# Optimization experiments

Measured on AMD Instinct MI355X. Metric: run time of the kernel, lower is better.

Reference implementation:

```python
import jax, jax.numpy as jnp
import numpy as np


def _pairwise_sq_dist(x, y):
    # x: [B, N, 3], y: [B, M, 3] -> P: [B, N, M] squared Euclidean distances
    xx = jnp.sum(x * x, axis=-1)                      # [B, N]
    yy = jnp.sum(y * y, axis=-1)                      # [B, M]
    zz = jnp.einsum('bnd,bmd->bnm', x, y)             # [B, N, M]
    return xx[:, :, None] + yy[:, None, :] - 2.0 * zz


def setup_inputs() -> dict:
    key = jax.random.key(0)
    k1, k2 = jax.random.split(key)
    B, K = 8, 8192
    adv_pc = jax.random.normal(k1, (B, K, 3), dtype=jnp.float32)
    ori_pc = jax.random.normal(k2, (B, K, 3), dtype=jnp.float32)
    weights = jnp.ones((B,), dtype=jnp.float32)
    return {"adv_pc": adv_pc, "ori_pc": ori_pc, "weights": weights}


def reference(adv_pc, ori_pc, weights):
    # P = pairwise_dist(gts=ori_pc, preds=adv_pc): [B, N_ori, N_adv]
    P = _pairwise_sq_dist(ori_pc, adv_pc)
    # method='adv2ori': loss1 = max over adv points of min over ori points
    loss1 = jnp.max(jnp.min(P, axis=1), axis=1)       # [B]
    loss = loss1 * weights
    return jnp.mean(loss)                             # batch_avg=True
```

## Files before the change

kernel.cpp:

```cpp
#include <hip/hip_runtime.h>


#define KPTS 8192
#define BATCH 8
#define NSPLIT 8
#define RBLK (KPTS / NSPLIT)
#define TSLICE (RBLK / 32)
#define CBLK 512
#define MCHUNK (KPTS / CBLK)

typedef _Float16 half8 __attribute__((ext_vector_type(8)));

#define TILE_ASM(af_, rm0_, rm1_, rm2_, rm3_, b0_, b1_, b2_, b3_)             \
    asm volatile(                                                             \
        "v_mfma_f32_32x32x16_f16 v[64:79], %4, %5, 0\n\t"                     \
        "v_mfma_f32_32x32x16_f16 v[80:95], %4, %6, 0\n\t"                     \
        "v_mfma_f32_32x32x16_f16 v[96:111], %4, %7, 0\n\t"                    \
        "v_mfma_f32_32x32x16_f16 v[112:127], %4, %8, 0\n\t"                   \
        "s_nop 7\n\t"                                                         \
        "s_nop 7\n\t"                                                         \
        "v_min3_f32 v64, v64, v65, v66\n\t"                                   \
        "v_min3_f32 v67, v67, v68, v69\n\t"                                   \
        "v_min3_f32 v70, v70, v71, v72\n\t"                                   \
        "v_min3_f32 v73, v73, v74, v75\n\t"                                   \
        "v_min3_f32 v76, v76, v77, v78\n\t"                                   \
        "v_min3_f32 v79, v79, %0, v64\n\t"                                    \
        "v_min3_f32 v67, v67, v70, v73\n\t"                                   \
        "v_min3_f32 %0, v76, v79, v67\n\t"                                    \
        "v_min3_f32 v80, v80, v81, v82\n\t"                                   \
        "v_min3_f32 v83, v83, v84, v85\n\t"                                   \
        "v_min3_f32 v86, v86, v87, v88\n\t"                                   \
        "v_min3_f32 v89, v89, v90, v91\n\t"                                   \
        "v_min3_f32 v92, v92, v93, v94\n\t"                                   \
        "v_min3_f32 v95, v95, %1, v80\n\t"                                    \
        "v_min3_f32 v83, v83, v86, v89\n\t"                                   \
        "v_min3_f32 %1, v92, v95, v83\n\t"                                    \
        "v_min3_f32 v96, v96, v97, v98\n\t"                                   \
        "v_min3_f32 v99, v99, v100, v101\n\t"                                 \
        "v_min3_f32 v102, v102, v103, v104\n\t"                               \
        "v_min3_f32 v105, v105, v106, v107\n\t"                               \
        "v_min3_f32 v108, v108, v109, v110\n\t"                               \
        "v_min3_f32 v111, v111, %2, v96\n\t"                                  \
        "v_min3_f32 v99, v99, v102, v105\n\t"                                 \
        "v_min3_f32 %2, v108, v111, v99\n\t"                                  \
        "v_min3_f32 v112, v112, v113, v114\n\t"                               \
        "v_min3_f32 v115, v115, v116, v117\n\t"                               \
        "v_min3_f32 v118, v118, v119, v120\n\t"                               \
        "v_min3_f32 v121, v121, v122, v123\n\t"                               \
        "v_min3_f32 v124, v124, v125, v126\n\t"                               \
        "v_min3_f32 v127, v127, %3, v112\n\t"                                 \
        "v_min3_f32 v115, v115, v118, v121\n\t"                               \
        "v_min3_f32 %3, v124, v127, v115"                                     \
        : "+v"(rm0_), "+v"(rm1_), "+v"(rm2_), "+v"(rm3_)                      \
        : "v"(af_), "v"(b0_), "v"(b1_), "v"(b2_), "v"(b3_)                    \
        : "v64","v65","v66","v67","v68","v69","v70","v71",                    \
          "v72","v73","v74","v75","v76","v77","v78","v79",                    \
          "v80","v81","v82","v83","v84","v85","v86","v87",                    \
          "v88","v89","v90","v91","v92","v93","v94","v95",                    \
          "v96","v97","v98","v99","v100","v101","v102","v103",                \
          "v104","v105","v106","v107","v108","v109","v110","v111",            \
          "v112","v113","v114","v115","v116","v117","v118","v119",            \
          "v120","v121","v122","v123","v124","v125","v126","v127")

__global__ __launch_bounds__(256, 4) void hausdorff(const float* __restrict__ adv,
                                                    const float* __restrict__ ori,
                                                    float* __restrict__ part,
                                                    float* __restrict__ out) {
    __shared__ _Float16 sA[(TSLICE + 1) * 512];

    const int bid  = blockIdx.x;
    const int b    = bid >> 7;
    const int mc   = (bid >> 3) & (MCHUNK - 1);
    const int ns   = bid & 7;
    const int tid  = threadIdx.x;
    const int lane = tid & 63;
    const int wv   = tid >> 6;
    const int r    = lane & 31;
    const int hk   = lane >> 5;

    if (bid == 0 && tid == 0) out[0] = 0.0f;

    const _Float16 Z = (_Float16)0.0f, ONE = (_Float16)1.0f;

    const float* advb = adv + (size_t)b * KPTS * 3;
    const int m0 = mc * CBLK + wv * 128 + r;
    half8 bf0, bf1, bf2, bf3;
    float aa0, aa1, aa2, aa3;
#pragma unroll
    for (int i = 0; i < 4; ++i) {
        const int m = m0 + 32 * i;
        float ax = advb[3 * m], ay = advb[3 * m + 1], az = advb[3 * m + 2];
        float aa = ax * ax + ay * ay + az * az;
        float tx = -2.f * ax, ty = -2.f * ay, tz = -2.f * az;
        _Float16 bx = (_Float16)tx, by = (_Float16)ty, bz = (_Float16)tz;
        _Float16 cx = (_Float16)(tx - (float)bx);
        _Float16 cy = (_Float16)(ty - (float)by);
        _Float16 cz = (_Float16)(tz - (float)bz);
        half8 h0 = {bx, by, bz, cx, cy, cz, bx, by};
        half8 h1 = {bz, ONE, ONE, Z, Z, Z, Z, Z};
        half8 bi = hk ? h1 : h0;
        if (i == 0) { bf0 = bi; aa0 = aa; }
        else if (i == 1) { bf1 = bi; aa1 = aa; }
        else if (i == 2) { bf2 = bi; aa2 = aa; }
        else { bf3 = bi; aa3 = aa; }
    }

    const float* orib = ori + ((size_t)b * KPTS + (size_t)ns * RBLK) * 3;
#pragma unroll
    for (int i = 0; i < 4; ++i) {
        const int rr = tid + i * 256;
        const float* op = orib + (size_t)rr * 3;
        float x = op[0], y = op[1], z = op[2];
        float oo = x * x + y * y + z * z;
        _Float16 hx = (_Float16)x, hy = (_Float16)y, hz = (_Float16)z;
        _Float16 lx = (_Float16)(x - (float)hx);
        _Float16 ly = (_Float16)(y - (float)hy);
        _Float16 lz = (_Float16)(z - (float)hz);
        _Float16 oh = (_Float16)oo;
        _Float16 ol = (_Float16)(oo - (float)oh);
        half8 a0 = {hx, hy, hz, hx, hy, hz, lx, ly};
        half8 a1 = {lz, oh, ol, Z, Z, Z, Z, Z};
        const int off = ((rr >> 5) << 9) + ((rr & 31) << 3);
        *(half8*)(&sA[off])       = a0;
        *(half8*)(&sA[off + 256]) = a1;
    }
    __syncthreads();

    float rm0 = __builtin_huge_valf(), rm1 = __builtin_huge_valf();
    float rm2 = __builtin_huge_valf(), rm3 = __builtin_huge_valf();

    const _Float16* apl = sA + lane * 8;

    half8 af = *(const half8*)apl;
#pragma unroll 2
    for (int t = 0; t < TSLICE; ++t) {
        half8 afn = *(const half8*)(apl + (size_t)(t + 1) * 512);
        TILE_ASM(af, rm0, rm1, rm2, rm3, bf0, bf1, bf2, bf3);
        af = afn;
    }

    rm0 = fminf(rm0, __shfl_xor(rm0, 32, 64));
    rm1 = fminf(rm1, __shfl_xor(rm1, 32, 64));
    rm2 = fminf(rm2, __shfl_xor(rm2, 32, 64));
    rm3 = fminf(rm3, __shfl_xor(rm3, 32, 64));

    float* p = part + ((size_t)ns * BATCH + b) * KPTS;
    if (hk == 0) {
        p[m0]      = fmaxf(rm0 + aa0, 0.0f);
        p[m0 + 32] = fmaxf(rm1 + aa1, 0.0f);
        p[m0 + 64] = fmaxf(rm2 + aa2, 0.0f);
        p[m0 + 96] = fmaxf(rm3 + aa3, 0.0f);
    }
}

__global__ __launch_bounds__(1024) void reduceB(const float* __restrict__ part,
                                                const float* __restrict__ w,
                                                float* __restrict__ out) {
    const int b = blockIdx.x;
    const int tid = threadIdx.x;

    float mx = 0.0f;
#pragma unroll
    for (int h = 0; h < 2; ++h) {
        const int c4 = tid + h * 1024;
        float4 v[NSPLIT];
#pragma unroll
        for (int s = 0; s < NSPLIT; ++s)
            v[s] = *(const float4*)(part + ((size_t)s * BATCH + b) * KPTS + (size_t)c4 * 4);
        float4 mn = v[0];
#pragma unroll
        for (int s = 1; s < NSPLIT; ++s) {
            mn.x = fminf(mn.x, v[s].x); mn.y = fminf(mn.y, v[s].y);
            mn.z = fminf(mn.z, v[s].z); mn.w = fminf(mn.w, v[s].w);
        }
        mx = fmaxf(mx, fmaxf(fmaxf(mn.x, mn.y), fmaxf(mn.z, mn.w)));
    }

#pragma unroll
    for (int off = 32; off; off >>= 1)
        mx = fmaxf(mx, __shfl_xor(mx, off, 64));

    __shared__ float red[16];
    if ((tid & 63) == 0) red[tid >> 6] = mx;
    __syncthreads();
    if (tid == 0) {
        float m2 = red[0];
#pragma unroll
        for (int i = 1; i < 16; ++i) m2 = fmaxf(m2, red[i]);
        atomicAdd(out, m2 * w[b] * (1.0f / BATCH));
    }
}

extern "C" void kernel_launch(void* const* d_in, const int* in_sizes, int n_in,
                              void* d_out, int out_size, void* d_ws, size_t ws_size,
                              hipStream_t stream) {
    const float* adv = (const float*)d_in[0];
    const float* ori = (const float*)d_in[1];
    const float* w   = (const float*)d_in[2];
    float* out = (float*)d_out;
    float* part = (float*)d_ws;

    hausdorff<<<BATCH * MCHUNK * NSPLIT, 256, 0, stream>>>(adv, ori, part, out);
    reduceB<<<BATCH, 1024, 0, stream>>>((const float*)part, w, out);
}
```

Before: 75.45 us.

## Software-pipeline MFMA tiles with min-folds across two accumulator halves

Splits the monolithic MFMA+min3 inline asm into separate MFMA and fold blocks for two register halves. The loop is rotated so each iteration folds the previous tile's X results before issuing new X MFMAs, then does the same for Y, with prologue and epilogue peeled. This is meant to hide MFMA latency behind the VALU min reductions and drop the per-iteration s_nop stalls. It relies on the compiler not touching the clobbered registers between the separate asm statements, which it is not formally required to honour.

```diff
diff --git a/kernel.cpp b/kernel.cpp
--- a/kernel.cpp
+++ b/kernel.cpp
@@ -11,14 +11,29 @@
 
 typedef _Float16 half8 __attribute__((ext_vector_type(8)));
 
-#define TILE_ASM(af_, rm0_, rm1_, rm2_, rm3_, b0_, b1_, b2_, b3_)             \
-    asm volatile(                                                             \
-        "v_mfma_f32_32x32x16_f16 v[64:79], %4, %5, 0\n\t"                     \
-        "v_mfma_f32_32x32x16_f16 v[80:95], %4, %6, 0\n\t"                     \
-        "v_mfma_f32_32x32x16_f16 v[96:111], %4, %7, 0\n\t"                    \
-        "v_mfma_f32_32x32x16_f16 v[112:127], %4, %8, 0\n\t"                   \
-        "s_nop 7\n\t"                                                         \
-        "s_nop 7\n\t"                                                         \
+#define CLOB_X "v64","v65","v66","v67","v68","v69","v70","v71",               \
+               "v72","v73","v74","v75","v76","v77","v78","v79",               \
+               "v80","v81","v82","v83","v84","v85","v86","v87",               \
+               "v88","v89","v90","v91","v92","v93","v94","v95"
+#define CLOB_Y "v96","v97","v98","v99","v100","v101","v102","v103",           \
+               "v104","v105","v106","v107","v108","v109","v110","v111",       \
+               "v112","v113","v114","v115","v116","v117","v118","v119",       \
+               "v120","v121","v122","v123","v124","v125","v126","v127"
+
+#define MFMA2_X(af_, b0_, b1_)                                                \
+    asm volatile(                                                             \
+        "v_mfma_f32_32x32x16_f16 v[64:79], %0, %1, 0\n\t"                     \
+        "v_mfma_f32_32x32x16_f16 v[80:95], %0, %2, 0"                         \
+        :: "v"(af_), "v"(b0_), "v"(b1_) : CLOB_X)
+
+#define MFMA2_Y(af_, b2_, b3_)                                                \
+    asm volatile(                                                             \
+        "v_mfma_f32_32x32x16_f16 v[96:111], %0, %1, 0\n\t"                    \
+        "v_mfma_f32_32x32x16_f16 v[112:127], %0, %2, 0"                       \
+        :: "v"(af_), "v"(b2_), "v"(b3_) : CLOB_Y)
+
+#define FOLD_X(rm0_, rm1_)                                                    \
+    asm volatile(                                                             \
         "v_min3_f32 v64, v64, v65, v66\n\t"                                   \
         "v_min3_f32 v67, v67, v68, v69\n\t"                                   \
         "v_min3_f32 v70, v70, v71, v72\n\t"                                   \
@@ -34,33 +49,28 @@
         "v_min3_f32 v92, v92, v93, v94\n\t"                                   \
         "v_min3_f32 v95, v95, %1, v80\n\t"                                    \
         "v_min3_f32 v83, v83, v86, v89\n\t"                                   \
-        "v_min3_f32 %1, v92, v95, v83\n\t"                                    \
+        "v_min3_f32 %1, v92, v95, v83"                                        \
+        : "+v"(rm0_), "+v"(rm1_) :: CLOB_X)
+
+#define FOLD_Y(rm2_, rm3_)                                                    \
+    asm volatile(                                                             \
         "v_min3_f32 v96, v96, v97, v98\n\t"                                   \
         "v_min3_f32 v99, v99, v100, v101\n\t"                                 \
         "v_min3_f32 v102, v102, v103, v104\n\t"                               \
         "v_min3_f32 v105, v105, v106, v107\n\t"                               \
         "v_min3_f32 v108, v108, v109, v110\n\t"                               \
-        "v_min3_f32 v111, v111, %2, v96\n\t"                                  \
+        "v_min3_f32 v111, v111, %0, v96\n\t"                                  \
         "v_min3_f32 v99, v99, v102, v105\n\t"                                 \
-        "v_min3_f32 %2, v108, v111, v99\n\t"                                  \
+        "v_min3_f32 %0, v108, v111, v99\n\t"                                  \
         "v_min3_f32 v112, v112, v113, v114\n\t"                               \
         "v_min3_f32 v115, v115, v116, v117\n\t"                               \
         "v_min3_f32 v118, v118, v119, v120\n\t"                               \
         "v_min3_f32 v121, v121, v122, v123\n\t"                               \
         "v_min3_f32 v124, v124, v125, v126\n\t"                               \
-        "v_min3_f32 v127, v127, %3, v112\n\t"                                 \
+        "v_min3_f32 v127, v127, %1, v112\n\t"                                 \
         "v_min3_f32 v115, v115, v118, v121\n\t"                               \
-        "v_min3_f32 %3, v124, v127, v115"                                     \
-        : "+v"(rm0_), "+v"(rm1_), "+v"(rm2_), "+v"(rm3_)                      \
-        : "v"(af_), "v"(b0_), "v"(b1_), "v"(b2_), "v"(b3_)                    \
-        : "v64","v65","v66","v67","v68","v69","v70","v71",                    \
-          "v72","v73","v74","v75","v76","v77","v78","v79",                    \
-          "v80","v81","v82","v83","v84","v85","v86","v87",                    \
-          "v88","v89","v90","v91","v92","v93","v94","v95",                    \
-          "v96","v97","v98","v99","v100","v101","v102","v103",                \
-          "v104","v105","v106","v107","v108","v109","v110","v111",            \
-          "v112","v113","v114","v115","v116","v117","v118","v119",            \
-          "v120","v121","v122","v123","v124","v125","v126","v127")
+        "v_min3_f32 %1, v124, v127, v115"                                     \
+        : "+v"(rm2_), "+v"(rm3_) :: CLOB_Y)
 
 __global__ __launch_bounds__(256, 4) void hausdorff(const float* __restrict__ adv,
                                                     const float* __restrict__ ori,
@@ -132,12 +142,23 @@
     const _Float16* apl = sA + lane * 8;
 
     half8 af = *(const half8*)apl;
+    MFMA2_X(af, bf0, bf1);
+    MFMA2_Y(af, bf2, bf3);
+    asm volatile("s_nop 7\n\ts_nop 7" ::: );
+    af = *(const half8*)(apl + 512);
+
 #pragma unroll 2
-    for (int t = 0; t < TSLICE; ++t) {
+    for (int t = 1; t < TSLICE; ++t) {
         half8 afn = *(const half8*)(apl + (size_t)(t + 1) * 512);
-        TILE_ASM(af, rm0, rm1, rm2, rm3, bf0, bf1, bf2, bf3);
+        FOLD_X(rm0, rm1);
+        MFMA2_X(af, bf0, bf1);
+        FOLD_Y(rm2, rm3);
+        MFMA2_Y(af, bf2, bf3);
         af = afn;
     }
+
+    FOLD_X(rm0, rm1);
+    FOLD_Y(rm2, rm3);
 
     rm0 = fminf(rm0, __shfl_xor(rm0, 32, 64));
     rm1 = fminf(rm1, __shfl_xor(rm1, 32, 64));
```

Result: slower. 77.26 us (+2.4%).
